# Kernel optimization log

Measured on AMD Instinct MI355X. Metric: run time of the kernel, lower is better.

Reference implementation:

```python
import jax, jax.numpy as jnp
import numpy as np

EMBED_DIM = 1024
NUM_HEADS = 16
HEAD_DIM = EMBED_DIM // NUM_HEADS


def setup_inputs() -> dict:
    key = jax.random.key(0)
    ks = jax.random.split(key, 9)
    B, S, D = 2, 2048, EMBED_DIM
    scale = 1.0 / np.sqrt(D)
    x = jax.random.normal(ks[0], (B, S, D), dtype=jnp.float32)
    # nn.Linear weights are [out, in]; store as [in, out] for x @ W
    Wq = jax.random.uniform(ks[1], (D, D), jnp.float32, -scale, scale)
    bq = jax.random.uniform(ks[2], (D,), jnp.float32, -scale, scale)
    Wk = jax.random.uniform(ks[3], (D, D), jnp.float32, -scale, scale)
    bk = jax.random.uniform(ks[4], (D,), jnp.float32, -scale, scale)
    Wv = jax.random.uniform(ks[5], (D, D), jnp.float32, -scale, scale)
    bv = jax.random.uniform(ks[6], (D,), jnp.float32, -scale, scale)
    Wo = jax.random.uniform(ks[7], (D, D), jnp.float32, -scale, scale)
    bo = jax.random.uniform(ks[8], (D,), jnp.float32, -scale, scale)
    return {"x": x, "Wq": Wq, "bq": bq, "Wk": Wk, "bk": bk,
            "Wv": Wv, "bv": bv, "Wo": Wo, "bo": bo}


def reference(x, Wq, bq, Wk, bk, Wv, bv, Wo, bo):
    B, S, D = x.shape
    H, Dh = NUM_HEADS, HEAD_DIM
    q = (x @ Wq + bq).reshape(B, S, H, Dh).transpose(0, 2, 1, 3)  # [B,H,S,Dh]
    k = (x @ Wk + bk).reshape(B, S, H, Dh).transpose(0, 2, 1, 3)
    v = (x @ Wv + bv).reshape(B, S, H, Dh).transpose(0, 2, 1, 3)
    scores = jnp.einsum('bhqd,bhkd->bhqk', q, k) / jnp.sqrt(jnp.float32(Dh))
    attn = jax.nn.softmax(scores, axis=-1)
    out = jnp.einsum('bhqk,bhkd->bhqd', attn, v)  # [B,H,S,Dh]
    out = out.transpose(0, 2, 1, 3).reshape(B, S, D)
    return out @ Wo + bo
```

## Files before the change

kernel.cpp:

```cpp
#include <hip/hip_runtime.h>
#include <hip/hip_bf16.h>
#include <stdint.h>

using f32x4 = __attribute__((ext_vector_type(4))) float;
using s16x8 = __attribute__((ext_vector_type(8))) short;
using s16x4 = __attribute__((ext_vector_type(4))) short;

__device__ __forceinline__ unsigned short f2bf(float f) {
  union { float f; unsigned int u; } v; v.f = f;
  return (unsigned short)((v.u + 0x7FFFu + ((v.u >> 16) & 1u)) >> 16);
}

__device__ __forceinline__ float exp2_(float x) {
  float r;
  asm("v_exp_f32 %0, %1" : "=v"(r) : "v"(x));
  return r;
}

__device__ __forceinline__ s16x4 pk4(float a, float b, float c, float d) {
  union { unsigned u[2]; s16x4 v; } r;
  asm("v_cvt_pk_bf16_f32 %0, %1, %2" : "=v"(r.u[0]) : "v"(a), "v"(b));
  asm("v_cvt_pk_bf16_f32 %0, %1, %2" : "=v"(r.u[1]) : "v"(c), "v"(d));
  return r.v;
}

__device__ __forceinline__ short pbf(float f) {
  __hip_bfloat16 h = __float2bfloat16(f);
  return *(short*)&h;
}

#define GLD16(gp, lp) __builtin_amdgcn_global_load_lds( \
    (const __attribute__((address_space(1))) unsigned int*)(uintptr_t)(gp), \
    (__attribute__((address_space(3))) unsigned int*)(uintptr_t)(lp), 16, 0, 0)

__device__ __forceinline__ f32x4 mfma32(s16x8 a, s16x8 b, f32x4 c) {
  return __builtin_amdgcn_mfma_f32_16x16x32_bf16(a, b, c, 0, 0, 0);
}

#if __has_builtin(__builtin_amdgcn_mfma_f32_16x16x16bf16_1k)
__device__ __forceinline__ f32x4 mfma16(s16x4 a, s16x4 b, f32x4 c) {
  return __builtin_amdgcn_mfma_f32_16x16x16bf16_1k(a, b, c, 0, 0, 0);
}
#else
__device__ __forceinline__ f32x4 mfma16(s16x4 a, s16x4 b, f32x4 c) {
  f32x4 d;
  asm volatile("v_mfma_f32_16x16x16_bf16 %0, %1, %2, %3"
               : "=v"(d) : "v"(a), "v"(b), "v"(c));
  return d;
}
#endif

__global__ __launch_bounds__(256)
void prep(const float* __restrict__ x,
          const float* __restrict__ Wq, const float* __restrict__ Wk,
          const float* __restrict__ Wv, const float* __restrict__ Wo,
          unsigned short* __restrict__ xb, unsigned short* __restrict__ Wt) {
  __shared__ float tile[64][65];
  int blk = blockIdx.x;
  int tid = threadIdx.x;
  if (blk < 1024) {
    const float4* xi = (const float4*)x;
    ushort4* xo = (ushort4*)xb;
    #pragma unroll
    for (int j = 0; j < 4; ++j) {
      int i = blk * 1024 + j * 256 + tid;
      float4 v = xi[i];
      ushort4 o;
      o.x = f2bf(v.x); o.y = f2bf(v.y); o.z = f2bf(v.z); o.w = f2bf(v.w);
      xo[i] = o;
    }
  } else {
    int wid = blk - 1024;
    int which = wid >> 8, t = wid & 255;
    const float* W = (which == 0) ? Wq : (which == 1) ? Wk : (which == 2) ? Wv : Wo;
    unsigned short* dst = Wt + (size_t)which * 1048576;
    int k0 = (t & 15) * 64, n0 = (t >> 4) * 64;
    int tx = tid & 63, ty = tid >> 6;
    #pragma unroll
    for (int j = 0; j < 64; j += 4)
      tile[ty + j][tx] = W[(size_t)(k0 + ty + j) * 1024 + n0 + tx];
    __syncthreads();
    #pragma unroll
    for (int j = 0; j < 64; j += 4)
      dst[(size_t)(n0 + ty + j) * 1024 + k0 + tx] = f2bf(tile[tx][ty + j]);
  }
}

__global__ __launch_bounds__(512, 2)
void qkv_gemm(const unsigned short* __restrict__ A,
              const unsigned short* __restrict__ Bt,
              const float* __restrict__ bq, const float* __restrict__ bk,
              const float* __restrict__ bv,
              unsigned short* __restrict__ qo, unsigned short* __restrict__ kf,
              unsigned short* __restrict__ vf) {
  __shared__ unsigned short lds2[2][32768];
  int orig = blockIdx.x;
  int wg = (orig & 7) * 24 + (orig >> 3);
  int bm = wg / 12, bn = wg % 12;
  int m0 = bm << 8, n0 = bn << 8;
  int tid = threadIdx.x;
  int w = tid >> 6, ln = tid & 63;
  int g = ln >> 4, c = ln & 15;
  int wm = w >> 2, wn = w & 3;

  int rrs = tid >> 3;
  int lcol = (((tid & 7) ^ ((tid >> 3) & 7)) << 4);
  const char* pA = (const char*)A + (size_t)(m0 + rrs) * 2048 + lcol;
  const char* pB = (const char*)Bt + (size_t)(n0 + rrs) * 2048 + lcol;
  int woff = w * 1024;

#define QKV_STAGE(buf, kt)                                                     \
  {                                                                            \
    char* db = (char*)&lds2[buf][0];                                           \
    _Pragma("unroll")                                                          \
    for (int h = 0; h < 2; ++h)                                                \
      _Pragma("unroll")                                                        \
      for (int i = 0; i < 2; ++i) {                                            \
        GLD16(pA + (size_t)(h * 128 + i * 64) * 2048 + (kt) * 128,             \
              db + h * 16384 + i * 8192 + woff);                               \
        GLD16(pB + (size_t)(h * 128 + i * 64) * 2048 + (kt) * 128,             \
              db + 32768 + h * 16384 + i * 8192 + woff);                       \
      }                                                                        \
  }

  int cs = (c & 7) << 4;
#define DSF(Lp, row, kk) \
  (*(const s16x8*)&(Lp)[(row) * 64 + ((((kk) * 64 + g * 16) ^ cs) >> 1)])

  f32x4 acc[8][4];
  f32x4 zero = {0.f, 0.f, 0.f, 0.f};
  #pragma unroll
  for (int mi = 0; mi < 8; ++mi)
    #pragma unroll
    for (int ni = 0; ni < 4; ++ni) acc[mi][ni] = zero;

  QKV_STAGE(0, 0);
  asm volatile("s_waitcnt vmcnt(0)" ::: "memory");
  __builtin_amdgcn_s_barrier();

  for (int kt = 0; kt < 16; ++kt) {
    int bsel = kt & 1;
    const unsigned short* LA = &lds2[bsel][wm * 8192];
    const unsigned short* LB = &lds2[bsel][16384 + (wn >> 1) * 8192];
    int rB = (wn & 1) * 64;
    if (kt < 15) QKV_STAGE(bsel ^ 1, kt + 1);

    s16x8 a[4][2], b0[2][2], b1[2][2];
    #pragma unroll
    for (int mi = 0; mi < 4; ++mi) {
      a[mi][0] = DSF(LA, mi * 16 + c, 0);
      a[mi][1] = DSF(LA, mi * 16 + c, 1);
    }
    #pragma unroll
    for (int ni = 0; ni < 2; ++ni) {
      b0[ni][0] = DSF(LB, rB + ni * 16 + c, 0);
      b0[ni][1] = DSF(LB, rB + ni * 16 + c, 1);
    }
    #pragma unroll
    for (int mi = 0; mi < 4; ++mi)
      #pragma unroll
      for (int ni = 0; ni < 2; ++ni) {
        acc[mi][ni] = mfma32(a[mi][0], b0[ni][0], acc[mi][ni]);
        acc[mi][ni] = mfma32(a[mi][1], b0[ni][1], acc[mi][ni]);
      }
    #pragma unroll
    for (int mi = 0; mi < 4; ++mi) {
      a[mi][0] = DSF(LA, (mi + 4) * 16 + c, 0);
      a[mi][1] = DSF(LA, (mi + 4) * 16 + c, 1);
    }
    #pragma unroll
    for (int mi = 0; mi < 4; ++mi)
      #pragma unroll
      for (int ni = 0; ni < 2; ++ni) {
        acc[mi + 4][ni] = mfma32(a[mi][0], b0[ni][0], acc[mi + 4][ni]);
        acc[mi + 4][ni] = mfma32(a[mi][1], b0[ni][1], acc[mi + 4][ni]);
      }
    #pragma unroll
    for (int ni = 0; ni < 2; ++ni) {
      b1[ni][0] = DSF(LB, rB + (ni + 2) * 16 + c, 0);
      b1[ni][1] = DSF(LB, rB + (ni + 2) * 16 + c, 1);
    }
    #pragma unroll
    for (int mi = 0; mi < 4; ++mi)
      #pragma unroll
      for (int ni = 0; ni < 2; ++ni) {
        acc[mi + 4][ni + 2] = mfma32(a[mi][0], b1[ni][0], acc[mi + 4][ni + 2]);
        acc[mi + 4][ni + 2] = mfma32(a[mi][1], b1[ni][1], acc[mi + 4][ni + 2]);
      }
    #pragma unroll
    for (int mi = 0; mi < 4; ++mi) {
      a[mi][0] = DSF(LA, mi * 16 + c, 0);
      a[mi][1] = DSF(LA, mi * 16 + c, 1);
    }
    #pragma unroll
    for (int mi = 0; mi < 4; ++mi)
      #pragma unroll
      for (int ni = 0; ni < 2; ++ni) {
        acc[mi][ni + 2] = mfma32(a[mi][0], b1[ni][0], acc[mi][ni + 2]);
        acc[mi][ni + 2] = mfma32(a[mi][1], b1[ni][1], acc[mi][ni + 2]);
      }

    asm volatile("s_waitcnt vmcnt(0)" ::: "memory");
    __builtin_amdgcn_s_barrier();
  }
#undef QKV_STAGE
#undef DSF

  #pragma unroll
  for (int ni = 0; ni < 4; ++ni) {
    int cg = n0 + wn * 64 + ni * 16 + c;
    int p = cg >> 10;
    int d = cg & 1023;
    int hh = d >> 6, dh = d & 63;
    const float* bp = (p == 0) ? bq : (p == 1) ? bk : bv;
    float bias = bp[d];
    #pragma unroll
    for (int mi = 0; mi < 8; ++mi) {
      int r = m0 + wm * 128 + mi * 16 + g * 4;
      int b2 = r >> 11, s = r & 2047;
      size_t pv = (size_t)((b2 << 4) + hh);
      if (p == 2) {
        int T = s >> 4;
        int Tp = T >> 1, par = T & 1;
        int dtp = dh >> 4;
        ushort4 pk;
        pk.x = f2bf(acc[mi][ni][0] + bias);
        pk.y = f2bf(acc[mi][ni][1] + bias);
        pk.z = f2bf(acc[mi][ni][2] + bias);
        pk.w = f2bf(acc[mi][ni][3] + bias);
        *(ushort4*)&vf[pv * 131072 +
                       (size_t)(((Tp * 4 + dtp) * 64 + g * 16 + c) * 8 + par * 4)] = pk;
      } else if (p == 1) {
        int T = s >> 4;
        int h2 = dh >> 5, gp = (dh >> 3) & 3, j = dh & 7;
        unsigned short* kd = kf + pv * 131072 + T * 1024 + h2 * 512 +
                             (gp * 16 + (s & 15)) * 8 + j;
        kd[0]  = f2bf(acc[mi][ni][0] + bias);
        kd[8]  = f2bf(acc[mi][ni][1] + bias);
        kd[16] = f2bf(acc[mi][ni][2] + bias);
        kd[24] = f2bf(acc[mi][ni][3] + bias);
      } else {
        const float sc = 0.180336880111120f;
        size_t base = (pv * 2048 + s) * 64 + dh;
        qo[base]       = f2bf((acc[mi][ni][0] + bias) * sc);
        qo[base + 64]  = f2bf((acc[mi][ni][1] + bias) * sc);
        qo[base + 128] = f2bf((acc[mi][ni][2] + bias) * sc);
        qo[base + 192] = f2bf((acc[mi][ni][3] + bias) * sc);
      }
    }
  }
}

__global__ __launch_bounds__(256, 2)
void attn_fwd(const unsigned short* __restrict__ q,
              const unsigned short* __restrict__ kfb,
              const unsigned short* __restrict__ vfb,
              unsigned short* __restrict__ ao) {
  __shared__ unsigned short ldsKV[3][8192];
  int orig = blockIdx.x;
  int wg = (orig & 7) * 64 + (orig >> 3);
  int pair = wg >> 4, qt = wg & 15;
  int tid = threadIdx.x;
  int w = tid >> 6, ln = tid & 63;
  int g = ln >> 4, c = ln & 15;
  int q0 = qt * 128 + w * 32;
  const unsigned short* qp = q + (size_t)pair * 131072;
  const char* kbase = (const char*)(kfb + (size_t)pair * 131072);
  const char* vbase = (const char*)(vfb + (size_t)pair * 131072);

  const char* ssrc = ((w < 2) ? kbase : vbase) + (w & 1) * 4096;
  int dsto = (w >= 2 ? 8192 : 0) + (w & 1) * 4096;

  s16x8 qf[2][2];
  #pragma unroll
  for (int j = 0; j < 2; ++j)
    #pragma unroll
    for (int h = 0; h < 2; ++h)
      qf[j][h] = *(const s16x8*)&qp[(q0 + j * 16 + c) * 64 + h * 32 + g * 8];

  f32x4 acc[2][4];
  f32x4 zero = {0.f, 0.f, 0.f, 0.f};
  #pragma unroll
  for (int j = 0; j < 2; ++j)
    #pragma unroll
    for (int dt = 0; dt < 4; ++dt) acc[j][dt] = zero;
  float l0 = 0.f, l1 = 0.f;

  #pragma unroll
  for (int j = 0; j < 4; ++j)
    GLD16(ssrc + j * 1024 + ln * 16, (char*)&ldsKV[0][0] + dsto + j * 1024);

  const unsigned short* L0 = ldsKV[0];
  const unsigned short* L1 = ldsKV[1];
  const unsigned short* L2 = ldsKV[2];
  s16x4 paA[2][4], paB[2][4];

#define ATTN_ITER(T, LC, LP, LN, PAC, PAP)                                     \
  {                                                                            \
    if ((T) < 31) {                                                            \
      const char* s2 = ssrc + ((T) + 1) * 8192;                                \
      char* d2 = (char*)(LN) + dsto;                                           \
      _Pragma("unroll")                                                        \
      for (int j = 0; j < 4; ++j)                                              \
        GLD16(s2 + j * 1024 + ln * 16, d2 + j * 1024);                         \
      asm volatile("s_waitcnt vmcnt(4)" ::: "memory");                         \
    } else {                                                                   \
      asm volatile("s_waitcnt vmcnt(0)" ::: "memory");                         \
    }                                                                          \
    __builtin_amdgcn_s_barrier();                                              \
    s16x8 kc[4][2];                                                            \
    _Pragma("unroll")                                                          \
    for (int kt = 0; kt < 4; ++kt) {                                           \
      kc[kt][0] = *(const s16x8*)&(LC)[kt * 1024 + ln * 8];                    \
      kc[kt][1] = *(const s16x8*)&(LC)[kt * 1024 + 512 + ln * 8];              \
    }                                                                          \
    f32x4 st[4][2];                                                            \
    __builtin_amdgcn_s_setprio(1);                                             \
    _Pragma("unroll")                                                          \
    for (int kt = 0; kt < 4; ++kt)                                             \
      _Pragma("unroll")                                                        \
      for (int j = 0; j < 2; ++j) {                                            \
        f32x4 t2 = zero;                                                       \
        t2 = mfma32(kc[kt][0], qf[j][0], t2);                                  \
        t2 = mfma32(kc[kt][1], qf[j][1], t2);                                  \
        st[kt][j] = t2;                                                        \
      }                                                                        \
    __builtin_amdgcn_s_setprio(0);                                             \
    if ((T) > 0) {                                                             \
      __builtin_amdgcn_s_setprio(1);                                           \
      _Pragma("unroll")                                                        \
      for (int dt = 0; dt < 4; ++dt)                                           \
        _Pragma("unroll")                                                      \
        for (int tp = 0; tp < 2; ++tp) {                                       \
          s16x8 vv = *(const s16x8*)&(LP)[4096 + tp * 2048 + dt * 512 + ln * 8]; \
          s16x4 vlo = __builtin_shufflevector(vv, vv, 0, 1, 2, 3);             \
          s16x4 vhi = __builtin_shufflevector(vv, vv, 4, 5, 6, 7);             \
          _Pragma("unroll")                                                    \
          for (int j = 0; j < 2; ++j) {                                        \
            acc[j][dt] = mfma16((PAP)[j][tp * 2], vlo, acc[j][dt]);            \
            acc[j][dt] = mfma16((PAP)[j][tp * 2 + 1], vhi, acc[j][dt]);        \
          }                                                                    \
        }                                                                      \
      __builtin_amdgcn_s_setprio(0);                                           \
    }                                                                          \
    _Pragma("unroll")                                                          \
    for (int kt = 0; kt < 4; ++kt) {                                           \
      float p00 = exp2_(st[kt][0][0]), p01 = exp2_(st[kt][0][1]);              \
      float p02 = exp2_(st[kt][0][2]), p03 = exp2_(st[kt][0][3]);              \
      float p10 = exp2_(st[kt][1][0]), p11 = exp2_(st[kt][1][1]);              \
      float p12 = exp2_(st[kt][1][2]), p13 = exp2_(st[kt][1][3]);              \
      l0 += (p00 + p01) + (p02 + p03);                                         \
      l1 += (p10 + p11) + (p12 + p13);                                         \
      (PAC)[0][kt] = pk4(p00, p01, p02, p03);                                  \
      (PAC)[1][kt] = pk4(p10, p11, p12, p13);                                  \
    }                                                                          \
    __builtin_amdgcn_s_barrier();                                              \
  }

  for (int t = 0; t < 32; t += 2) {
    ATTN_ITER(t,     L0, L2, L1, paA, paB);
    ATTN_ITER(t + 1, L1, L0, L2, paB, paA);
    const unsigned short* tmp = L2;
    L2 = L1; L1 = L0; L0 = tmp;
  }
#undef ATTN_ITER

  __builtin_amdgcn_s_setprio(1);
  #pragma unroll
  for (int dt = 0; dt < 4; ++dt)
    #pragma unroll
    for (int tp = 0; tp < 2; ++tp) {
      s16x8 vv = *(const s16x8*)&L2[4096 + tp * 2048 + dt * 512 + ln * 8];
      s16x4 vlo = __builtin_shufflevector(vv, vv, 0, 1, 2, 3);
      s16x4 vhi = __builtin_shufflevector(vv, vv, 4, 5, 6, 7);
      #pragma unroll
      for (int j = 0; j < 2; ++j) {
        acc[j][dt] = mfma16(paB[j][tp * 2], vlo, acc[j][dt]);
        acc[j][dt] = mfma16(paB[j][tp * 2 + 1], vhi, acc[j][dt]);
      }
    }
  __builtin_amdgcn_s_setprio(0);

  l0 += __shfl_xor(l0, 16); l0 += __shfl_xor(l0, 32);
  l1 += __shfl_xor(l1, 16); l1 += __shfl_xor(l1, 32);
  float li0 = 1.f / l0, li1 = 1.f / l1;
  int b = pair >> 4, hh = pair & 15;
  #pragma unroll
  for (int e = 0; e < 4; ++e) {
    float i0 = __shfl(li0, g * 4 + e);
    float i1 = __shfl(li1, g * 4 + e);
    size_t r0 = ((size_t)(b * 2048 + q0 + g * 4 + e) * 16 + hh) * 64;
    size_t r1 = ((size_t)(b * 2048 + q0 + 16 + g * 4 + e) * 16 + hh) * 64;
    #pragma unroll
    for (int dt = 0; dt < 4; ++dt) {
      ao[r0 + dt * 16 + c] = (unsigned short)pbf(acc[0][dt][e] * i0);
      ao[r1 + dt * 16 + c] = (unsigned short)pbf(acc[1][dt][e] * i1);
    }
  }
}

__global__ __launch_bounds__(256)
void out_gemm(const unsigned short* __restrict__ A,
              const unsigned short* __restrict__ Bt,
              const float* __restrict__ bo, float* __restrict__ out) {
  __shared__ unsigned short lds[2][6144];
  int orig = blockIdx.x;
  int wg = (orig & 7) * 64 + (orig >> 3);
  int bm = wg >> 3, bn = wg & 7;
  int m0 = bm << 6, n0 = bn << 7;
  int tid = threadIdx.x;
  int w = tid >> 6, ln = tid & 63;
  int g = ln >> 4, c = ln & 15;
  int wr = w >> 1, wc = w & 1;

  const unsigned short* su[3];
  int du[3];
  #pragma unroll
  for (int i = 0; i < 3; ++i) {
    int u = 3 * w + i;
    if (u < 4) {
      su[i] = A + (size_t)(m0 + u * 16 + (ln >> 2)) * 1024 + (ln & 3) * 8;
      du[i] = u * 512;
    } else {
      int v2 = u - 4;
      su[i] = Bt + (size_t)(n0 + v2 * 16 + (ln >> 2)) * 1024 + (ln & 3) * 8;
      du[i] = 2048 + v2 * 512;
    }
  }

  f32x4 acc[2][4];
  f32x4 zero = {0.f, 0.f, 0.f, 0.f};
  #pragma unroll
  for (int m = 0; m < 2; ++m)
    #pragma unroll
    for (int n = 0; n < 4; ++n) acc[m][n] = zero;

  #pragma unroll
  for (int i = 0; i < 3; ++i) GLD16(su[i], &lds[0][du[i]]);
  __syncthreads();

  int aoff = (wr * 32 + c) * 32 + g * 8;
  int boff = 2048 + (wc * 64 + c) * 32 + g * 8;

  int cur = 0;
  for (int t = 0; t < 32; ++t) {
    if (t < 31) {
      int nb = cur ^ 1;
      #pragma unroll
      for (int i = 0; i < 3; ++i) GLD16(su[i] + (t + 1) * 32, &lds[nb][du[i]]);
    }
    s16x8 af[2], bf[4];
    #pragma unroll
    for (int m = 0; m < 2; ++m)
      af[m] = *(const s16x8*)&lds[cur][aoff + m * 512];
    #pragma unroll
    for (int n = 0; n < 4; ++n)
      bf[n] = *(const s16x8*)&lds[cur][boff + n * 512];
    #pragma unroll
    for (int m = 0; m < 2; ++m)
      #pragma unroll
      for (int n = 0; n < 4; ++n)
        acc[m][n] = mfma32(af[m], bf[n], acc[m][n]);
    __syncthreads();
    cur ^= 1;
  }

  #pragma unroll
  for (int n = 0; n < 4; ++n) {
    int cg = n0 + wc * 64 + n * 16 + c;
    float bias = bo[cg];
    #pragma unroll
    for (int m = 0; m < 2; ++m) {
      int r = m0 + wr * 32 + m * 16 + g * 4;
      out[(size_t)r * 1024 + cg] = acc[m][n][0] + bias;
      out[(size_t)(r + 1) * 1024 + cg] = acc[m][n][1] + bias;
      out[(size_t)(r + 2) * 1024 + cg] = acc[m][n][2] + bias;
      out[(size_t)(r + 3) * 1024 + cg] = acc[m][n][3] + bias;
    }
  }
}

extern "C" void kernel_launch(void* const* d_in, const int* in_sizes, int n_in,
                              void* d_out, int out_size, void* d_ws, size_t ws_size,
                              hipStream_t stream) {
  (void)in_sizes; (void)n_in; (void)out_size; (void)ws_size;
  const float* x  = (const float*)d_in[0];
  const float* Wq = (const float*)d_in[1];
  const float* bq = (const float*)d_in[2];
  const float* Wk = (const float*)d_in[3];
  const float* bk = (const float*)d_in[4];
  const float* Wv = (const float*)d_in[5];
  const float* bv = (const float*)d_in[6];
  const float* Wo = (const float*)d_in[7];
  const float* bo = (const float*)d_in[8];
  float* out = (float*)d_out;
  char* ws = (char*)d_ws;
  unsigned short* xb  = (unsigned short*)(ws);
  unsigned short* Wt  = (unsigned short*)(ws + 8388608);
  unsigned short* Wot = (unsigned short*)(ws + 14680064);
  unsigned short* qb  = (unsigned short*)(ws + 16777216);
  unsigned short* kfb = (unsigned short*)(ws + 25165824);
  unsigned short* vfb = (unsigned short*)(ws + 33554432);
  unsigned short* ao  = (unsigned short*)(ws + 41943040);

  prep<<<2048, 256, 0, stream>>>(x, Wq, Wk, Wv, Wo, xb, Wt);
  qkv_gemm<<<192, 512, 0, stream>>>(xb, Wt, bq, bk, bv, qb, kfb, vfb);
  attn_fwd<<<512, 256, 0, stream>>>(qb, kfb, vfb, ao);
  out_gemm<<<512, 256, 0, stream>>>(ao, Wot, bo, out);
}
```

Measured before the change: 105.1 us.

## Retile QKV GEMM to 256x192 tiles so 256 workgroups fill all CUs

Shrinks the QKV GEMM's N-tile from 256 to 192 columns, which raises the grid from 192 to 256 workgroups to match the mi355x's 256 CUs and avoid idle units. LDS staging, fragment addressing and per-wave tiling are reworked so each wave computes 8x3 MFMA tiles with B fragments loaded once per k-step. s_setprio is also raised around the MFMA blocks to favour the matrix issue. Smaller tiles lower arithmetic intensity per workgroup, and the bias/epilogue indexing must handle 192-wide boundaries that cross Q/K/V splits.

```diff
diff --git a/kernel.cpp b/kernel.cpp
--- a/kernel.cpp
+++ b/kernel.cpp
@@ -93,11 +93,12 @@
               const float* __restrict__ bv,
               unsigned short* __restrict__ qo, unsigned short* __restrict__ kf,
               unsigned short* __restrict__ vf) {
-  __shared__ unsigned short lds2[2][32768];
+  __shared__ unsigned short lds2[2][28672];
   int orig = blockIdx.x;
-  int wg = (orig & 7) * 24 + (orig >> 3);
-  int bm = wg / 12, bn = wg % 12;
-  int m0 = bm << 8, n0 = bn << 8;
+  int wg = (orig & 7) * 32 + (orig >> 3);
+  int bm = wg >> 4, bn = wg & 15;
+  int m0 = bm << 8;
+  int n0 = bn * 192;
   int tid = threadIdx.x;
   int w = tid >> 6, ln = tid & 63;
   int g = ln >> 4, c = ln & 15;
@@ -113,26 +114,29 @@
   {                                                                            \
     char* db = (char*)&lds2[buf][0];                                           \
     _Pragma("unroll")                                                          \
-    for (int h = 0; h < 2; ++h)                                                \
-      _Pragma("unroll")                                                        \
-      for (int i = 0; i < 2; ++i) {                                            \
-        GLD16(pA + (size_t)(h * 128 + i * 64) * 2048 + (kt) * 128,             \
-              db + h * 16384 + i * 8192 + woff);                               \
-        GLD16(pB + (size_t)(h * 128 + i * 64) * 2048 + (kt) * 128,             \
-              db + 32768 + h * 16384 + i * 8192 + woff);                       \
-      }                                                                        \
+    for (int s = 0; s < 4; ++s)                                                \
+      GLD16(pA + (size_t)s * 131072 + (kt) * 128, db + s * 8192 + woff);       \
+    _Pragma("unroll")                                                          \
+    for (int s = 0; s < 3; ++s)                                                \
+      GLD16(pB + (size_t)s * 131072 + (kt) * 128,                              \
+            db + 32768 + s * 8192 + woff);                                     \
   }
 
   int cs = (c & 7) << 4;
-#define DSF(Lp, row, kk) \
-  (*(const s16x8*)&(Lp)[(row) * 64 + ((((kk) * 64 + g * 16) ^ cs) >> 1)])
-
-  f32x4 acc[8][4];
+#define DSFA(LA, mi, kk)                                                       \
+  (*(const s16x8*)&(LA)[((mi) >> 2) * 4096 + (((mi) & 3) * 16 + c) * 64 +      \
+                        ((((kk) * 64 + g * 16) ^ cs) >> 1)])
+#define DSFB(LB, ni, kk)                                                       \
+  (*(const s16x8*)&(LB)[((wn * 48 + (ni) * 16) >> 6) * 4096 +                  \
+                        (((wn * 48 + (ni) * 16) & 63) + c) * 64 +              \
+                        ((((kk) * 64 + g * 16) ^ cs) >> 1)])
+
+  f32x4 acc[8][3];
   f32x4 zero = {0.f, 0.f, 0.f, 0.f};
   #pragma unroll
   for (int mi = 0; mi < 8; ++mi)
     #pragma unroll
-    for (int ni = 0; ni < 4; ++ni) acc[mi][ni] = zero;
+    for (int ni = 0; ni < 3; ++ni) acc[mi][ni] = zero;
 
   QKV_STAGE(0, 0);
   asm volatile("s_waitcnt vmcnt(0)" ::: "memory");
@@ -141,74 +145,55 @@
   for (int kt = 0; kt < 16; ++kt) {
     int bsel = kt & 1;
     const unsigned short* LA = &lds2[bsel][wm * 8192];
-    const unsigned short* LB = &lds2[bsel][16384 + (wn >> 1) * 8192];
-    int rB = (wn & 1) * 64;
+    const unsigned short* LB = &lds2[bsel][16384];
     if (kt < 15) QKV_STAGE(bsel ^ 1, kt + 1);
 
-    s16x8 a[4][2], b0[2][2], b1[2][2];
+    s16x8 bfr[3][2];
+    #pragma unroll
+    for (int ni = 0; ni < 3; ++ni) {
+      bfr[ni][0] = DSFB(LB, ni, 0);
+      bfr[ni][1] = DSFB(LB, ni, 1);
+    }
+    s16x8 a[4][2];
     #pragma unroll
     for (int mi = 0; mi < 4; ++mi) {
-      a[mi][0] = DSF(LA, mi * 16 + c, 0);
-      a[mi][1] = DSF(LA, mi * 16 + c, 1);
-    }
-    #pragma unroll
-    for (int ni = 0; ni < 2; ++ni) {
-      b0[ni][0] = DSF(LB, rB + ni * 16 + c, 0);
-      b0[ni][1] = DSF(LB, rB + ni * 16 + c, 1);
-    }
+      a[mi][0] = DSFA(LA, mi, 0);
+      a[mi][1] = DSFA(LA, mi, 1);
+    }
+    __builtin_amdgcn_s_setprio(1);
     #pragma unroll
     for (int mi = 0; mi < 4; ++mi)
       #pragma unroll
-      for (int ni = 0; ni < 2; ++ni) {
-        acc[mi][ni] = mfma32(a[mi][0], b0[ni][0], acc[mi][ni]);
-        acc[mi][ni] = mfma32(a[mi][1], b0[ni][1], acc[mi][ni]);
+      for (int ni = 0; ni < 3; ++ni) {
+        acc[mi][ni] = mfma32(a[mi][0], bfr[ni][0], acc[mi][ni]);
+        acc[mi][ni] = mfma32(a[mi][1], bfr[ni][1], acc[mi][ni]);
       }
+    __builtin_amdgcn_s_setprio(0);
     #pragma unroll
     for (int mi = 0; mi < 4; ++mi) {
-      a[mi][0] = DSF(LA, (mi + 4) * 16 + c, 0);
-      a[mi][1] = DSF(LA, (mi + 4) * 16 + c, 1);
-    }
+      a[mi][0] = DSFA(LA, mi + 4, 0);
+      a[mi][1] = DSFA(LA, mi + 4, 1);
+    }
+    __builtin_amdgcn_s_setprio(1);
     #pragma unroll
     for (int mi = 0; mi < 4; ++mi)
       #pragma unroll
-      for (int ni = 0; ni < 2; ++ni) {
-        acc[mi + 4][ni] = mfma32(a[mi][0], b0[ni][0], acc[mi + 4][ni]);
-        acc[mi + 4][ni] = mfma32(a[mi][1], b0[ni][1], acc[mi + 4][ni]);
+      for (int ni = 0; ni < 3; ++ni) {
+        acc[mi + 4][ni] = mfma32(a[mi][0], bfr[ni][0], acc[mi + 4][ni]);
+        acc[mi + 4][ni] = mfma32(a[mi][1], bfr[ni][1], acc[mi + 4][ni]);
       }
-    #pragma unroll
-    for (int ni = 0; ni < 2; ++ni) {
-      b1[ni][0] = DSF(LB, rB + (ni + 2) * 16 + c, 0);
-      b1[ni][1] = DSF(LB, rB + (ni + 2) * 16 + c, 1);
-    }
-    #pragma unroll
-    for (int mi = 0; mi < 4; ++mi)
-      #pragma unroll
-      for (int ni = 0; ni < 2; ++ni) {
-        acc[mi + 4][ni + 2] = mfma32(a[mi][0], b1[ni][0], acc[mi + 4][ni + 2]);
-        acc[mi + 4][ni + 2] = mfma32(a[mi][1], b1[ni][1], acc[mi + 4][ni + 2]);
-      }
-    #pragma unroll
-    for (int mi = 0; mi < 4; ++mi) {
-      a[mi][0] = DSF(LA, mi * 16 + c, 0);
-      a[mi][1] = DSF(LA, mi * 16 + c, 1);
-    }
-    #pragma unroll
-    for (int mi = 0; mi < 4; ++mi)
-      #pragma unroll
-      for (int ni = 0; ni < 2; ++ni) {
-        acc[mi][ni + 2] = mfma32(a[mi][0], b1[ni][0], acc[mi][ni + 2]);
-        acc[mi][ni + 2] = mfma32(a[mi][1], b1[ni][1], acc[mi][ni + 2]);
-      }
+    __builtin_amdgcn_s_setprio(0);
 
     asm volatile("s_waitcnt vmcnt(0)" ::: "memory");
     __builtin_amdgcn_s_barrier();
   }
 #undef QKV_STAGE
-#undef DSF
-
-  #pragma unroll
-  for (int ni = 0; ni < 4; ++ni) {
-    int cg = n0 + wn * 64 + ni * 16 + c;
+#undef DSFA
+#undef DSFB
+
+  #pragma unroll
+  for (int ni = 0; ni < 3; ++ni) {
+    int cg = n0 + wn * 48 + ni * 16 + c;
     int p = cg >> 10;
     int d = cg & 1023;
     int hh = d >> 6, dh = d & 63;
@@ -504,7 +489,7 @@
   unsigned short* ao  = (unsigned short*)(ws + 41943040);
 
   prep<<<2048, 256, 0, stream>>>(x, Wq, Wk, Wv, Wo, xb, Wt);
-  qkv_gemm<<<192, 512, 0, stream>>>(xb, Wt, bq, bk, bv, qb, kfb, vfb);
+  qkv_gemm<<<256, 512, 0, stream>>>(xb, Wt, bq, bk, bv, qb, kfb, vfb);
   attn_fwd<<<512, 256, 0, stream>>>(qb, kfb, vfb, ao);
   out_gemm<<<512, 256, 0, stream>>>(ao, Wot, bo, out);
 }
```

After: 103.8 us. No clear change (-1.2%).
